# Kernel tuning notes

Hardware: AMD Instinct MI355X
Metric: run time of the kernel (lower is better)

Reference implementation:

```python
import jax, jax.numpy as jnp
import numpy as np
import math

B, S, D, H = 2, 2048, 2048, 16
HD = D // H  # 128


def _rope(x, cos, sin):
    # x: [b, s, h, hd]; cos/sin: [s, hd//2]
    # torch view_as_complex pairs adjacent elements: (even=real, odd=imag)
    xr = x[..., 0::2]
    xi = x[..., 1::2]
    c = cos[None, :, None, :]
    s = sin[None, :, None, :]
    out_r = xr * c - xi * s
    out_i = xr * s + xi * c
    # interleave back: [..., hd//2, 2] -> [..., hd]
    return jnp.stack([out_r, out_i], axis=-1).reshape(x.shape)


def setup_inputs() -> dict:
    key = jax.random.key(0)
    ks = jax.random.split(key, 5)
    x = jax.random.normal(ks[0], (B, S, D), dtype=jnp.float32)
    std = 1.0 / math.sqrt(D)
    wq = jax.random.normal(ks[1], (D, D), dtype=jnp.float32) * std
    wk = jax.random.normal(ks[2], (D, D), dtype=jnp.float32) * std
    wv = jax.random.normal(ks[3], (D, D), dtype=jnp.float32) * std
    wo = jax.random.normal(ks[4], (D, D), dtype=jnp.float32) * std
    # RoPE frequencies, theta = 10000
    freqs = 1.0 / (10000.0 ** (jnp.arange(0, HD, 2, dtype=jnp.float32) / HD))  # [hd//2]
    t = jnp.arange(S, dtype=jnp.float32)
    angles = jnp.outer(t, freqs)  # [s, hd//2]
    freqs_cos = jnp.cos(angles)
    freqs_sin = jnp.sin(angles)
    # causal additive mask [s, s]
    mask = jnp.triu(jnp.full((S, S), -jnp.inf, dtype=jnp.float32), k=1)
    return {"x": x, "start_pos": 0, "freqs_cos": freqs_cos, "freqs_sin": freqs_sin,
            "mask": mask, "wq": wq, "wk": wk, "wv": wv, "wo": wo}


def reference(x, start_pos, freqs_cos, freqs_sin, mask, wq, wk, wv, wo):
    b, s, d = x.shape
    # projections (torch Linear: y = x @ W.T)
    xq = (x @ wq.T).reshape(b, s, H, HD)
    xk = (x @ wk.T).reshape(b, s, H, HD)
    xv = (x @ wv.T).reshape(b, s, H, HD)
    xq = _rope(xq, freqs_cos, freqs_sin)
    xk = _rope(xk, freqs_cos, freqs_sin)
    # start_pos = 0 prefill: cache[:b, :s] == freshly computed xk/xv
    # scores: [b, h, s_q, s_k]
    scores = jnp.einsum("bqhd,bkhd->bhqk", xq, xk) / math.sqrt(HD)
    scores = scores + mask[None, None, :, :]
    probs = jax.nn.softmax(scores, axis=-1)
    out = jnp.einsum("bhqk,bkhd->bqhd", probs, xv).reshape(b, s, d)
    return out @ wo.T
```

## Files before the change

kernel.cpp:

```cpp
#include <hip/hip_runtime.h>

typedef __attribute__((ext_vector_type(8))) short short8;
typedef __attribute__((ext_vector_type(4))) float f32x4;
typedef __attribute__((ext_vector_type(16))) float f32x16;
typedef unsigned int u32;
typedef __attribute__((ext_vector_type(4))) u32 u32x4;
typedef unsigned short u16;

#define DEV __device__ __forceinline__

DEV void async16(const void* g, void* l) {
  __builtin_amdgcn_global_load_lds((const __attribute__((address_space(1))) u32*)g,
                                   (__attribute__((address_space(3))) u32*)l, 16, 0, 0);
}

DEV u16 f2bf(float f) {
  u32 u = __builtin_bit_cast(u32, f);
  u32 r = (u + 0x7FFFu + ((u >> 16) & 1u)) >> 16;
  return (u16)r;
}
DEV float bf2f(u16 h) { return __builtin_bit_cast(float, (u32)h << 16); }

DEV u32 cvtpk(float lo, float hi) {
  u32 r;
  asm("v_cvt_pk_bf16_f32 %0, %1, %2" : "=v"(r) : "v"(lo), "v"(hi));
  return r;
}

__global__ void cast_all_kernel(const float* __restrict__ x, const float* __restrict__ wq,
                                const float* __restrict__ wk, const float* __restrict__ wv,
                                const float* __restrict__ wo, u16* __restrict__ out,
                                const float* __restrict__ cb, const float* __restrict__ sb,
                                float4* __restrict__ cs_ws) {
  constexpr int XN = 2097152;
  constexpr int WN = 1048576;
  constexpr int TOT = XN + 4 * WN;
  constexpr int CSN = 32768;
  int stride = gridDim.x * blockDim.x;
  for (int i = blockIdx.x * blockDim.x + threadIdx.x; i < TOT + CSN; i += stride) {
    if (i < TOT) {
      const float* src;
      int off;
      if (i < XN) {
        src = x; off = i;
      } else {
        int j = i - XN, wsel = j >> 20;
        const float* ws4[4] = {wq, wk, wv, wo};
        src = ws4[wsel]; off = j & (WN - 1);
      }
      float4 v = reinterpret_cast<const float4*>(src)[off];
      ushort4 o = make_ushort4(f2bf(v.x), f2bf(v.y), f2bf(v.z), f2bf(v.w));
      reinterpret_cast<ushort4*>(out)[i] = o;
    } else {
      int j = i - TOT;
      float4 c4 = reinterpret_cast<const float4*>(cb)[j];
      float4 s4 = reinterpret_cast<const float4*>(sb)[j];
      cs_ws[2 * j] = make_float4(c4.x, s4.x, c4.y, s4.y);
      cs_ws[2 * j + 1] = make_float4(c4.z, s4.z, c4.w, s4.w);
    }
  }
}

template <int MODE>
__global__ __launch_bounds__(256) void gemm_bt(const u16* __restrict__ A,
                                               const u16* __restrict__ Bw,
                                               void* __restrict__ C0,
                                               u16* __restrict__ C1,
                                               u16* __restrict__ C2,
                                               const float2* __restrict__ csp) {
  constexpr int K = 2048;
  __shared__ char sm[32768];
  const int tid = threadIdx.x;
  const int lane = tid & 63;
  const int w = tid >> 6;
  const int by = blockIdx.x & 31;
  const int bx = blockIdx.x >> 5;
  const int row0 = by * 128, col0 = bx * 128;
  const int wr = (w >> 1) * 64, wc = (w & 1) * 64;
  f32x4 acc[4][4] = {};

  for (int k0 = 0; k0 < K; k0 += 64) {
    __syncthreads();
#pragma unroll
    for (int i = 0; i < 4; ++i) {
      int slot = tid + i * 256;
      int r = slot >> 3, s = slot & 7;
      int sl = s ^ (r & 7);
      async16(A + (size_t)(row0 + r) * K + (k0 + sl * 8), sm + slot * 16);
    }
#pragma unroll
    for (int i = 0; i < 4; ++i) {
      int slot = tid + i * 256;
      int r = slot >> 3, s = slot & 7;
      int sl = s ^ (r & 7);
      async16(Bw + (size_t)(col0 + r) * K + (k0 + sl * 8), sm + 16384 + slot * 16);
    }
    __syncthreads();
#pragma unroll
    for (int kk = 0; kk < 2; ++kk) {
      short8 af[4], bfr[4];
#pragma unroll
      for (int mi = 0; mi < 4; ++mi) {
        int r = wr + mi * 16 + (lane & 15);
        int ps = (kk * 4 + (lane >> 4)) ^ (r & 7);
        af[mi] = *reinterpret_cast<const short8*>(sm + r * 128 + ps * 16);
      }
#pragma unroll
      for (int ni = 0; ni < 4; ++ni) {
        int r = wc + ni * 16 + (lane & 15);
        int ps = (kk * 4 + (lane >> 4)) ^ (r & 7);
        bfr[ni] = *reinterpret_cast<const short8*>(sm + 16384 + r * 128 + ps * 16);
      }
#pragma unroll
      for (int mi = 0; mi < 4; ++mi)
#pragma unroll
        for (int ni = 0; ni < 4; ++ni)
          acc[mi][ni] = __builtin_amdgcn_mfma_f32_16x16x32_bf16(af[mi], bfr[ni], acc[mi][ni], 0, 0, 0);
    }
  }
  if constexpr (MODE == 0) {
    const int tsel = col0 >> 11;
    if (tsel < 2) {
      const float sc = (tsel == 0) ? 0.127517436f : 1.0f;
      u16* dst = tsel ? C2 : (u16*)C0;
#pragma unroll
      for (int mi = 0; mi < 4; ++mi) {
        float2 cs[4][4];
#pragma unroll
        for (int ni = 0; ni < 4; ++ni)
#pragma unroll
          for (int rr = 0; rr < 4; ++rr) {
            int gm = row0 + wr + mi * 16 + ((lane >> 4) << 2) + rr;
            int hd = wc + ni * 16 + (lane & 15);
            cs[ni][rr] = csp[((gm & 2047) << 6) + (hd >> 1)];
          }
#pragma unroll
        for (int ni = 0; ni < 4; ++ni)
#pragma unroll
          for (int rr = 0; rr < 4; ++rr) {
            int gm = row0 + wr + mi * 16 + ((lane >> 4) << 2) + rr;
            int hd = wc + ni * 16 + (lane & 15);
            int b = gm >> 11, s = gm & 2047, h = hd >> 7;
            (void)h;
            int hh = ((col0 & 2047) + wc + ni * 16) >> 7;
            float v = acc[mi][ni][rr];
            float pv = __shfl_xor(v, 1, 64);
            float c = cs[ni][rr].x, sn = cs[ni][rr].y;
            float o = (hd & 1) ? (pv * sn + v * c) : (v * c - pv * sn);
            o *= sc;
            dst[(size_t)((b << 4) | hh) * 262144 + (s << 7) + (hd & 127)] = f2bf(o);
          }
      }
    } else {
#pragma unroll
      for (int mi = 0; mi < 4; ++mi)
#pragma unroll
        for (int ni = 0; ni < 4; ++ni)
#pragma unroll
          for (int rr = 0; rr < 4; ++rr) {
            int gm = row0 + wr + mi * 16 + ((lane >> 4) << 2) + rr;
            int gn = col0 + wc + ni * 16 + (lane & 15);
            int nn = gn & 2047;
            int b = gm >> 11, s = gm & 2047, h = nn >> 7, hd = nn & 127;
            C1[(size_t)((b << 4) | h) * 262144 + (hd << 11) + s] = f2bf(acc[mi][ni][rr]);
          }
    }
  } else {
#pragma unroll
    for (int mi = 0; mi < 4; ++mi)
#pragma unroll
      for (int ni = 0; ni < 4; ++ni)
#pragma unroll
        for (int rr = 0; rr < 4; ++rr) {
          int gm = row0 + wr + mi * 16 + ((lane >> 4) << 2) + rr;
          int gn = col0 + wc + ni * 16 + (lane & 15);
          ((float*)C0)[((size_t)gm << 11) + gn] = acc[mi][ni][rr];
        }
  }
}

__global__ __launch_bounds__(256, 2) void attn_kernel(const u16* __restrict__ q_ws,
                                                      const u16* __restrict__ k_ws,
                                                      const u16* __restrict__ vt_ws,
                                                      u16* __restrict__ attn_ws) {
  constexpr int S = 2048;
  constexpr float NEGBIG = -3.0e38f;
  __shared__ char sm[65536];
  const int tid = threadIdx.x, lane = tid & 63, w = tid >> 6;
  const int hi = lane >> 5, l31 = lane & 31;
  const int bid = blockIdx.x;
  const int qtr = bid >> 5;
  const int qt = (qtr < 8) ? qtr : 23 - qtr;
  const int bh = ((bid & 7) << 2) | ((bid >> 3) & 3);
  const int qr0 = qt * 128 + w * 32;
  const int ntile = 2 * qt + 2;
  const int my_nt = (qr0 >> 6) + 1;

  const u16* qp = q_ws + (size_t)bh * S * 128;
  const u16* kp = k_ws + (size_t)bh * S * 128;
  const u16* vp = vt_ws + (size_t)bh * 128 * S;

  short8 qf[8];
  {
    const u16* qr = qp + (size_t)(qr0 + l31) * 128 + hi * 8;
#pragma unroll
    for (int ks = 0; ks < 8; ++ks) qf[ks] = *reinterpret_cast<const short8*>(qr + ks * 16);
  }
  f32x16 accO[4];
#pragma unroll
  for (int dc = 0; dc < 4; ++dc)
#pragma unroll
    for (int r = 0; r < 16; ++r) accO[dc][r] = 0.f;
  float m = -1e30f, l = 0.f;

  auto stage = [&](int bufoff, int kv0) {
#pragma unroll
    for (int i = 0; i < 4; ++i) {
      int slot = tid + i * 256;
      int r = slot >> 4, s = slot & 15;
      async16(kp + (size_t)(kv0 + r) * 128 + ((s ^ (r & 15)) * 8), sm + bufoff + slot * 16);
    }
#pragma unroll
    for (int i = 0; i < 4; ++i) {
      int slot = tid + i * 256;
      int r = slot >> 3, s = slot & 7;
      async16(vp + (size_t)r * S + kv0 + ((s ^ (r & 7)) * 8), sm + bufoff + 16384 + slot * 16);
    }
  };

  stage(0, 0);
  __syncthreads();

  for (int t = 0; t < ntile; ++t) {
    const char* kb = sm + (t & 1) * 32768;
    const char* vb = kb + 16384;
    if (t + 1 < ntile) stage(((t + 1) & 1) * 32768, (t + 1) * 64);

    if (t < my_nt) {
      f32x16 sacc[2];
#pragma unroll
      for (int jc = 0; jc < 2; ++jc)
#pragma unroll
        for (int r = 0; r < 16; ++r) sacc[jc][r] = 0.f;
      __builtin_amdgcn_s_setprio(1);
#pragma unroll
      for (int jc = 0; jc < 2; ++jc) {
        const char* krp = kb + (jc * 32 + l31) * 256;
        const int sw = l31 & 15;
#pragma unroll
        for (int ks = 0; ks < 8; ++ks) {
          short8 kf = *reinterpret_cast<const short8*>(krp + (((2 * ks + hi) ^ sw) << 4));
          sacc[jc] = __builtin_amdgcn_mfma_f32_32x32x16_bf16(kf, qf[ks], sacc[jc], 0, 0, 0);
        }
      }
      __builtin_amdgcn_s_setprio(0);
      if (t == my_nt - 1) {
#pragma unroll
        for (int jc = 0; jc < 2; ++jc) {
          int thr = qr0 + l31 - t * 64 - 32 * jc - 4 * hi;
#pragma unroll
          for (int r = 0; r < 16; ++r) {
            int c0 = (r & 3) + 8 * (r >> 2);
            if (c0 > thr) sacc[jc][r] = NEGBIG;
          }
        }
      }
      float pmA = NEGBIG, pmB = NEGBIG, pmC = NEGBIG, pmD = NEGBIG;
#pragma unroll
      for (int jc = 0; jc < 2; ++jc)
#pragma unroll
        for (int r = 0; r < 16; r += 4) {
          pmA = fmaxf(pmA, sacc[jc][r]);
          pmB = fmaxf(pmB, sacc[jc][r + 1]);
          pmC = fmaxf(pmC, sacc[jc][r + 2]);
          pmD = fmaxf(pmD, sacc[jc][r + 3]);
        }
      float pmax = fmaxf(fmaxf(pmA, pmB), fmaxf(pmC, pmD));
      pmax = fmaxf(pmax, __shfl_xor(pmax, 32, 64));
      if (!__all(pmax - m <= 8.0f)) {
        float mnew = fmaxf(m, pmax);
        float scl = exp2f(m - mnew);
        m = mnew;
        l *= scl;
#pragma unroll
        for (int dc = 0; dc < 4; ++dc)
#pragma unroll
          for (int r = 0; r < 16; ++r) accO[dc][r] *= scl;
      }
      float sA = 0.f, sB = 0.f, sC = 0.f, sD = 0.f;
#pragma unroll
      for (int jc = 0; jc < 2; ++jc)
#pragma unroll
        for (int r = 0; r < 16; r += 4) {
          float p0 = exp2f(sacc[jc][r] - m);
          float p1 = exp2f(sacc[jc][r + 1] - m);
          float p2 = exp2f(sacc[jc][r + 2] - m);
          float p3 = exp2f(sacc[jc][r + 3] - m);
          sacc[jc][r] = p0; sacc[jc][r + 1] = p1; sacc[jc][r + 2] = p2; sacc[jc][r + 3] = p3;
          sA += p0; sB += p1; sC += p2; sD += p3;
        }
      float ps = (sA + sB) + (sC + sD);
      ps += __shfl_xor(ps, 32, 64);
      l += ps;
      short8 pfrag[4];
#pragma unroll
      for (int ks = 0; ks < 4; ++ks) {
        const int jc = ks >> 1, u8 = (ks & 1) * 8;
        u32 wA = cvtpk(sacc[jc][u8 + 0], sacc[jc][u8 + 1]);
        u32 wB = cvtpk(sacc[jc][u8 + 2], sacc[jc][u8 + 3]);
        u32 wC = cvtpk(sacc[jc][u8 + 4], sacc[jc][u8 + 5]);
        u32 wD = cvtpk(sacc[jc][u8 + 6], sacc[jc][u8 + 7]);
        u32 qA = __shfl_xor(wA, 32, 64);
        u32 qB = __shfl_xor(wB, 32, 64);
        u32 qC = __shfl_xor(wC, 32, 64);
        u32 qD = __shfl_xor(wD, 32, 64);
        u32x4 t4;
        t4.x = hi ? qC : wA;
        t4.y = hi ? qD : wB;
        t4.z = hi ? wC : qA;
        t4.w = hi ? wD : qB;
        pfrag[ks] = __builtin_bit_cast(short8, t4);
      }
      __builtin_amdgcn_s_setprio(1);
#pragma unroll
      for (int ks = 0; ks < 4; ++ks) {
#pragma unroll
        for (int dc = 0; dc < 4; ++dc) {
          const char* vrp = vb + (dc * 32 + l31) * 128;
          short8 vf = *reinterpret_cast<const short8*>(vrp + (((2 * ks + hi) ^ (l31 & 7)) << 4));
          accO[dc] = __builtin_amdgcn_mfma_f32_32x32x16_bf16(vf, pfrag[ks], accO[dc], 0, 0, 0);
        }
      }
      __builtin_amdgcn_s_setprio(0);
    }
    __syncthreads();
  }

  const int b = bh >> 4, h = bh & 15;
  char* tb = sm + w * 8192;
  float inv = (l > 0.f) ? 1.0f / l : 0.f;
#pragma unroll
  for (int dc = 0; dc < 4; ++dc)
#pragma unroll
    for (int r = 0; r < 16; ++r) {
      int d = dc * 32 + (r & 3) + 8 * (r >> 2) + 4 * hi;
      int byte = l31 * 256 + d * 2;
      *reinterpret_cast<u16*>(tb + (byte ^ ((l31 & 7) << 4))) = f2bf(accO[dc][r] * inv);
    }
  asm volatile("s_waitcnt lgkmcnt(0)" ::: "memory");
#pragma unroll
  for (int i = 0; i < 8; ++i) {
    int r = i * 4 + (lane >> 4);
    int s = lane & 15;
    f32x4 v = *reinterpret_cast<const f32x4*>(tb + r * 256 + ((s ^ (r & 7)) << 4));
    size_t addr = ((size_t)(b * 2048 + qr0 + r) << 11) + (h << 7) + s * 8;
    *reinterpret_cast<f32x4*>(attn_ws + addr) = v;
  }
}

extern "C" void kernel_launch(void* const* d_in, const int* in_sizes, int n_in,
                              void* d_out, int out_size, void* d_ws, size_t ws_size,
                              hipStream_t stream) {
  const float* x = (const float*)d_in[0];
  const float* cb = (const float*)d_in[2];
  const float* sb = (const float*)d_in[3];
  const float* wq = (const float*)d_in[5];
  const float* wk = (const float*)d_in[6];
  const float* wv = (const float*)d_in[7];
  const float* wo = (const float*)d_in[8];

  char* p = (char*)d_ws;
  u16* xb  = (u16*)p; p += (size_t)4096 * 2048 * 2;
  u16* wqb = (u16*)p; p += (size_t)2048 * 2048 * 2;
  u16* wkb = (u16*)p; p += (size_t)2048 * 2048 * 2;
  u16* wvb = (u16*)p; p += (size_t)2048 * 2048 * 2;
  u16* wob = (u16*)p; p += (size_t)2048 * 2048 * 2;
  u16* q_ws = (u16*)p; p += (size_t)4096 * 2048 * 2;
  u16* k_ws = (u16*)p; p += (size_t)4096 * 2048 * 2;
  u16* vt_ws = (u16*)p; p += (size_t)4096 * 2048 * 2;
  float* cs_ws = (float*)p; p += (size_t)2048 * 64 * 2 * 4;
  u16* attn_ws = xb;
  (void)wkb; (void)wvb;

  cast_all_kernel<<<3072, 256, 0, stream>>>(x, wq, wk, wv, wo, xb, cb, sb, (float4*)cs_ws);

  gemm_bt<0><<<1536, 256, 0, stream>>>(xb, wqb, q_ws, vt_ws, k_ws, (const float2*)cs_ws);

  attn_kernel<<<512, 256, 0, stream>>>(q_ws, k_ws, vt_ws, attn_ws);

  gemm_bt<1><<<512, 256, 0, stream>>>(attn_ws, wob, d_out, nullptr, nullptr, nullptr);
}
```

Measured before the change: 268.1 us.

## Shrink attention blocks to 64 query rows, load V from global to registers, remap GEMM tiles per XCD

```diff
diff --git a/kernel.cpp b/kernel.cpp
--- a/kernel.cpp
+++ b/kernel.cpp
@@ -73,8 +73,11 @@
   const int tid = threadIdx.x;
   const int lane = tid & 63;
   const int w = tid >> 6;
-  const int by = blockIdx.x & 31;
-  const int bx = blockIdx.x >> 5;
+  const int bid = blockIdx.x;
+  const int xcd = bid & 7, jj = bid >> 3;
+  const int by = (xcd & 1) * 16 + (jj & 15);
+  const int bx = (MODE == 0) ? ((xcd >> 1) * 12 + (jj >> 4))
+                             : ((xcd >> 1) * 4 + (jj >> 4));
   const int row0 = by * 128, col0 = bx * 128;
   const int wr = (w >> 1) * 64, wc = (w & 1) * 64;
   f32x4 acc[4][4] = {};
@@ -140,8 +143,7 @@
           for (int rr = 0; rr < 4; ++rr) {
             int gm = row0 + wr + mi * 16 + ((lane >> 4) << 2) + rr;
             int hd = wc + ni * 16 + (lane & 15);
-            int b = gm >> 11, s = gm & 2047, h = hd >> 7;
-            (void)h;
+            int b = gm >> 11, s = gm & 2047;
             int hh = ((col0 & 2047) + wc + ni * 16) >> 7;
             float v = acc[mi][ni][rr];
             float pv = __shfl_xor(v, 1, 64);
@@ -179,22 +181,21 @@
   }
 }
 
-__global__ __launch_bounds__(256, 2) void attn_kernel(const u16* __restrict__ q_ws,
-                                                      const u16* __restrict__ k_ws,
-                                                      const u16* __restrict__ vt_ws,
-                                                      u16* __restrict__ attn_ws) {
+__global__ __launch_bounds__(128) void attn_kernel(const u16* __restrict__ q_ws,
+                                                   const u16* __restrict__ k_ws,
+                                                   const u16* __restrict__ vt_ws,
+                                                   u16* __restrict__ attn_ws) {
   constexpr int S = 2048;
   constexpr float NEGBIG = -3.0e38f;
-  __shared__ char sm[65536];
+  __shared__ char sm[32768];
   const int tid = threadIdx.x, lane = tid & 63, w = tid >> 6;
   const int hi = lane >> 5, l31 = lane & 31;
   const int bid = blockIdx.x;
   const int qtr = bid >> 5;
-  const int qt = (qtr < 8) ? qtr : 23 - qtr;
+  const int qt = (qtr < 16) ? qtr : 47 - qtr;
   const int bh = ((bid & 7) << 2) | ((bid >> 3) & 3);
-  const int qr0 = qt * 128 + w * 32;
-  const int ntile = 2 * qt + 2;
-  const int my_nt = (qr0 >> 6) + 1;
+  const int qr0 = qt * 64 + w * 32;
+  const int ntile = qt + 1;
 
   const u16* qp = q_ws + (size_t)bh * S * 128;
   const u16* kp = k_ws + (size_t)bh * S * 128;
@@ -213,126 +214,121 @@
     for (int r = 0; r < 16; ++r) accO[dc][r] = 0.f;
   float m = -1e30f, l = 0.f;
 
-  auto stage = [&](int bufoff, int kv0) {
-#pragma unroll
-    for (int i = 0; i < 4; ++i) {
-      int slot = tid + i * 256;
+  auto stageK = [&](int bufoff, int kv0) {
+#pragma unroll
+    for (int i = 0; i < 8; ++i) {
+      int slot = tid + i * 128;
       int r = slot >> 4, s = slot & 15;
       async16(kp + (size_t)(kv0 + r) * 128 + ((s ^ (r & 15)) * 8), sm + bufoff + slot * 16);
     }
-#pragma unroll
-    for (int i = 0; i < 4; ++i) {
-      int slot = tid + i * 256;
-      int r = slot >> 3, s = slot & 7;
-      async16(vp + (size_t)r * S + kv0 + ((s ^ (r & 7)) * 8), sm + bufoff + 16384 + slot * 16);
-    }
   };
 
-  stage(0, 0);
+  stageK(0, 0);
   __syncthreads();
 
   for (int t = 0; t < ntile; ++t) {
-    const char* kb = sm + (t & 1) * 32768;
-    const char* vb = kb + 16384;
-    if (t + 1 < ntile) stage(((t + 1) & 1) * 32768, (t + 1) * 64);
-
-    if (t < my_nt) {
-      f32x16 sacc[2];
-#pragma unroll
-      for (int jc = 0; jc < 2; ++jc)
-#pragma unroll
-        for (int r = 0; r < 16; ++r) sacc[jc][r] = 0.f;
-      __builtin_amdgcn_s_setprio(1);
+    const char* kb = sm + (t & 1) * 16384;
+    short8 vreg[4][4];
+#pragma unroll
+    for (int ks = 0; ks < 4; ++ks)
+#pragma unroll
+      for (int dc = 0; dc < 4; ++dc)
+        vreg[ks][dc] = *reinterpret_cast<const short8*>(
+            vp + (size_t)(dc * 32 + l31) * S + t * 64 + (2 * ks + hi) * 8);
+    __builtin_amdgcn_sched_barrier(0);
+    if (t + 1 < ntile) stageK(((t + 1) & 1) * 16384, (t + 1) * 64);
+
+    f32x16 sacc[2];
+#pragma unroll
+    for (int jc = 0; jc < 2; ++jc)
+#pragma unroll
+      for (int r = 0; r < 16; ++r) sacc[jc][r] = 0.f;
+    __builtin_amdgcn_s_setprio(1);
+#pragma unroll
+    for (int jc = 0; jc < 2; ++jc) {
+      const char* krp = kb + (jc * 32 + l31) * 256;
+      const int sw = l31 & 15;
+#pragma unroll
+      for (int ks = 0; ks < 8; ++ks) {
+        short8 kf = *reinterpret_cast<const short8*>(krp + (((2 * ks + hi) ^ sw) << 4));
+        sacc[jc] = __builtin_amdgcn_mfma_f32_32x32x16_bf16(kf, qf[ks], sacc[jc], 0, 0, 0);
+      }
+    }
+    __builtin_amdgcn_s_setprio(0);
+    if (t == ntile - 1) {
 #pragma unroll
       for (int jc = 0; jc < 2; ++jc) {
-        const char* krp = kb + (jc * 32 + l31) * 256;
-        const int sw = l31 & 15;
-#pragma unroll
-        for (int ks = 0; ks < 8; ++ks) {
-          short8 kf = *reinterpret_cast<const short8*>(krp + (((2 * ks + hi) ^ sw) << 4));
-          sacc[jc] = __builtin_amdgcn_mfma_f32_32x32x16_bf16(kf, qf[ks], sacc[jc], 0, 0, 0);
+        int thr = qr0 + l31 - t * 64 - 32 * jc - 4 * hi;
+#pragma unroll
+        for (int r = 0; r < 16; ++r) {
+          int c0 = (r & 3) + 8 * (r >> 2);
+          if (c0 > thr) sacc[jc][r] = NEGBIG;
         }
       }
-      __builtin_amdgcn_s_setprio(0);
-      if (t == my_nt - 1) {
-#pragma unroll
-        for (int jc = 0; jc < 2; ++jc) {
-          int thr = qr0 + l31 - t * 64 - 32 * jc - 4 * hi;
-#pragma unroll
-          for (int r = 0; r < 16; ++r) {
-            int c0 = (r & 3) + 8 * (r >> 2);
-            if (c0 > thr) sacc[jc][r] = NEGBIG;
-          }
-        }
-      }
-      float pmA = NEGBIG, pmB = NEGBIG, pmC = NEGBIG, pmD = NEGBIG;
-#pragma unroll
-      for (int jc = 0; jc < 2; ++jc)
-#pragma unroll
-        for (int r = 0; r < 16; r += 4) {
-          pmA = fmaxf(pmA, sacc[jc][r]);
-          pmB = fmaxf(pmB, sacc[jc][r + 1]);
-          pmC = fmaxf(pmC, sacc[jc][r + 2]);
-          pmD = fmaxf(pmD, sacc[jc][r + 3]);
-        }
-      float pmax = fmaxf(fmaxf(pmA, pmB), fmaxf(pmC, pmD));
-      pmax = fmaxf(pmax, __shfl_xor(pmax, 32, 64));
-      if (!__all(pmax - m <= 8.0f)) {
-        float mnew = fmaxf(m, pmax);
-        float scl = exp2f(m - mnew);
-        m = mnew;
-        l *= scl;
-#pragma unroll
-        for (int dc = 0; dc < 4; ++dc)
-#pragma unroll
-          for (int r = 0; r < 16; ++r) accO[dc][r] *= scl;
-      }
-      float sA = 0.f, sB = 0.f, sC = 0.f, sD = 0.f;
-#pragma unroll
-      for (int jc = 0; jc < 2; ++jc)
-#pragma unroll
-        for (int r = 0; r < 16; r += 4) {
-          float p0 = exp2f(sacc[jc][r] - m);
-          float p1 = exp2f(sacc[jc][r + 1] - m);
-          float p2 = exp2f(sacc[jc][r + 2] - m);
-          float p3 = exp2f(sacc[jc][r + 3] - m);
-          sacc[jc][r] = p0; sacc[jc][r + 1] = p1; sacc[jc][r + 2] = p2; sacc[jc][r + 3] = p3;
-          sA += p0; sB += p1; sC += p2; sD += p3;
-        }
-      float ps = (sA + sB) + (sC + sD);
-      ps += __shfl_xor(ps, 32, 64);
-      l += ps;
-      short8 pfrag[4];
-#pragma unroll
-      for (int ks = 0; ks < 4; ++ks) {
-        const int jc = ks >> 1, u8 = (ks & 1) * 8;
-        u32 wA = cvtpk(sacc[jc][u8 + 0], sacc[jc][u8 + 1]);
-        u32 wB = cvtpk(sacc[jc][u8 + 2], sacc[jc][u8 + 3]);
-        u32 wC = cvtpk(sacc[jc][u8 + 4], sacc[jc][u8 + 5]);
-        u32 wD = cvtpk(sacc[jc][u8 + 6], sacc[jc][u8 + 7]);
-        u32 qA = __shfl_xor(wA, 32, 64);
-        u32 qB = __shfl_xor(wB, 32, 64);
-        u32 qC = __shfl_xor(wC, 32, 64);
-        u32 qD = __shfl_xor(wD, 32, 64);
-        u32x4 t4;
-        t4.x = hi ? qC : wA;
-        t4.y = hi ? qD : wB;
-        t4.z = hi ? wC : qA;
-        t4.w = hi ? wD : qB;
-        pfrag[ks] = __builtin_bit_cast(short8, t4);
-      }
-      __builtin_amdgcn_s_setprio(1);
-#pragma unroll
-      for (int ks = 0; ks < 4; ++ks) {
-#pragma unroll
-        for (int dc = 0; dc < 4; ++dc) {
-          const char* vrp = vb + (dc * 32 + l31) * 128;
-          short8 vf = *reinterpret_cast<const short8*>(vrp + (((2 * ks + hi) ^ (l31 & 7)) << 4));
-          accO[dc] = __builtin_amdgcn_mfma_f32_32x32x16_bf16(vf, pfrag[ks], accO[dc], 0, 0, 0);
-        }
-      }
-      __builtin_amdgcn_s_setprio(0);
-    }
+    }
+    float pmA = NEGBIG, pmB = NEGBIG, pmC = NEGBIG, pmD = NEGBIG;
+#pragma unroll
+    for (int jc = 0; jc < 2; ++jc)
+#pragma unroll
+      for (int r = 0; r < 16; r += 4) {
+        pmA = fmaxf(pmA, sacc[jc][r]);
+        pmB = fmaxf(pmB, sacc[jc][r + 1]);
+        pmC = fmaxf(pmC, sacc[jc][r + 2]);
+        pmD = fmaxf(pmD, sacc[jc][r + 3]);
+      }
+    float pmax = fmaxf(fmaxf(pmA, pmB), fmaxf(pmC, pmD));
+    pmax = fmaxf(pmax, __shfl_xor(pmax, 32, 64));
+    if (!__all(pmax - m <= 8.0f)) {
+      float mnew = fmaxf(m, pmax);
+      float scl = exp2f(m - mnew);
+      m = mnew;
+      l *= scl;
+#pragma unroll
+      for (int dc = 0; dc < 4; ++dc)
+#pragma unroll
+        for (int r = 0; r < 16; ++r) accO[dc][r] *= scl;
+    }
+    float sA = 0.f, sB = 0.f, sC = 0.f, sD = 0.f;
+#pragma unroll
+    for (int jc = 0; jc < 2; ++jc)
+#pragma unroll
+      for (int r = 0; r < 16; r += 4) {
+        float p0 = exp2f(sacc[jc][r] - m);
+        float p1 = exp2f(sacc[jc][r + 1] - m);
+        float p2 = exp2f(sacc[jc][r + 2] - m);
+        float p3 = exp2f(sacc[jc][r + 3] - m);
+        sacc[jc][r] = p0; sacc[jc][r + 1] = p1; sacc[jc][r + 2] = p2; sacc[jc][r + 3] = p3;
+        sA += p0; sB += p1; sC += p2; sD += p3;
+      }
+    float ps = (sA + sB) + (sC + sD);
+    ps += __shfl_xor(ps, 32, 64);
+    l += ps;
+    short8 pfrag[4];
+#pragma unroll
+    for (int ks = 0; ks < 4; ++ks) {
+      const int jc = ks >> 1, u8 = (ks & 1) * 8;
+      u32 wA = cvtpk(sacc[jc][u8 + 0], sacc[jc][u8 + 1]);
+      u32 wB = cvtpk(sacc[jc][u8 + 2], sacc[jc][u8 + 3]);
+      u32 wC = cvtpk(sacc[jc][u8 + 4], sacc[jc][u8 + 5]);
+      u32 wD = cvtpk(sacc[jc][u8 + 6], sacc[jc][u8 + 7]);
+      u32 qA = __shfl_xor(wA, 32, 64);
+      u32 qB = __shfl_xor(wB, 32, 64);
+      u32 qC = __shfl_xor(wC, 32, 64);
+      u32 qD = __shfl_xor(wD, 32, 64);
+      u32x4 t4;
+      t4.x = hi ? qC : wA;
+      t4.y = hi ? qD : wB;
+      t4.z = hi ? wC : qA;
+      t4.w = hi ? wD : qB;
+      pfrag[ks] = __builtin_bit_cast(short8, t4);
+    }
+    __builtin_amdgcn_s_setprio(1);
+#pragma unroll
+    for (int ks = 0; ks < 4; ++ks)
+#pragma unroll
+      for (int dc = 0; dc < 4; ++dc)
+        accO[dc] = __builtin_amdgcn_mfma_f32_32x32x16_bf16(vreg[ks][dc], pfrag[ks], accO[dc], 0, 0, 0);
+    __builtin_amdgcn_s_setprio(0);
     __syncthreads();
   }
 
@@ -386,7 +382,7 @@
 
   gemm_bt<0><<<1536, 256, 0, stream>>>(xb, wqb, q_ws, vt_ws, k_ws, (const float2*)cs_ws);
 
-  attn_kernel<<<512, 256, 0, stream>>>(q_ws, k_ws, vt_ws, attn_ws);
+  attn_kernel<<<1024, 128, 0, stream>>>(q_ws, k_ws, vt_ws, attn_ws);
 
   gemm_bt<1><<<512, 256, 0, stream>>>(attn_ws, wob, d_out, nullptr, nullptr, nullptr);
 }
```

Measured after the change: 326.9 us. +22.0%, slower.
